# Performance work log

Hardware: AMD Instinct MI355X
Metric: run time of the kernel (lower is better)

Reference implementation:

```python
import jax, jax.numpy as jnp
import numpy as np

B, L, HID = 4, 1024, 2048
H, DK, DV, KS = 16, 128, 128, 4
KEY_DIM, VAL_DIM = H * DK, H * DV
CONV_DIM = 2 * KEY_DIM + VAL_DIM
EPS = 1e-6


def setup_inputs() -> dict:
    key = jax.random.key(0)
    ks = jax.random.split(key, 8)
    return {
        "hidden_states": jax.random.normal(ks[0], (B, L, HID), jnp.float32),
        "W_qkvz": jax.random.normal(ks[1], (HID, 2 * KEY_DIM + 2 * VAL_DIM), jnp.float32) * 0.02,
        "W_ba": jax.random.normal(ks[2], (HID, 2 * H), jnp.float32) * 0.02,
        "conv_w": jax.random.normal(ks[3], (CONV_DIM, KS), jnp.float32) * 0.1,
        "conv_b": jnp.zeros((CONV_DIM,), jnp.float32),
        "A_log": jnp.log(jax.random.uniform(ks[4], (H,), jnp.float32, 1e-3, 16.0)),
        "dt_bias": jnp.ones((H,), jnp.float32),
        "norm_w": jnp.ones((DV,), jnp.float32),
        "W_out": jax.random.normal(ks[5], (VAL_DIM, HID), jnp.float32) * 0.02,
    }


def _l2norm(x):
    return x * jax.lax.rsqrt(jnp.sum(x * x, -1, keepdims=True) + EPS)


def _gdn_core(q, k, v, g, beta):
    # q,k: [B,L,H,DK], v: [B,L,H,DV], g,beta: [B,L,H]
    scale = q.shape[-1] ** -0.5

    def step(S, inp):
        qt, kt, vt, gt, bt = inp  # [B,H,*]
        S = S * jnp.exp(gt)[..., None, None]          # per-step gated decay
        v_pred = jnp.einsum('bhk,bhkd->bhd', kt, S)   # read memory at k_t
        delta = (vt - v_pred) * bt[..., None]         # delta-rule update
        S = S + jnp.einsum('bhk,bhd->bhkd', kt, delta)
        o = jnp.einsum('bhk,bhkd->bhd', qt, S) * scale
        return S, o

    S0 = jnp.zeros((q.shape[0], q.shape[2], q.shape[3], v.shape[3]), q.dtype)
    xs = (q.transpose(1, 0, 2, 3), k.transpose(1, 0, 2, 3), v.transpose(1, 0, 2, 3),
          g.transpose(1, 0, 2), beta.transpose(1, 0, 2))
    _, o = jax.lax.scan(step, S0, xs)
    return o.transpose(1, 0, 2, 3)  # [B,L,H,DV]


def reference(hidden_states, W_qkvz, W_ba, conv_w, conv_b, A_log, dt_bias, norm_w, W_out):
    qkvz = hidden_states @ W_qkvz                      # [B,L,2*key+2*val]
    ba = hidden_states @ W_ba                          # [B,L,2H]
    mixed = qkvz[..., :CONV_DIM]
    z = qkvz[..., CONV_DIM:].reshape(B, L, H, DV)
    b_, a_ = ba[..., :H], ba[..., H:]

    # depthwise causal conv1d (left pad KS-1), no activation (activation=None)
    x = mixed.transpose(0, 2, 1)                       # [B,C,L]
    x = jax.lax.conv_general_dilated(
        x, conv_w[:, None, :], (1,), [(KS - 1, 0)],
        dimension_numbers=('NCH', 'OIH', 'NCH'), feature_group_count=CONV_DIM)
    x = (x + conv_b[None, :, None]).transpose(0, 2, 1)  # [B,L,C]

    q = _l2norm(x[..., :KEY_DIM].reshape(B, L, H, DK))
    k = _l2norm(x[..., KEY_DIM:2 * KEY_DIM].reshape(B, L, H, DK))
    v = x[..., 2 * KEY_DIM:].reshape(B, L, H, DV)

    g = -jnp.exp(A_log)[None, None, :] * jax.nn.softplus(a_ + dt_bias[None, None, :])
    beta = jax.nn.sigmoid(b_)

    o = _gdn_core(q, k, v, g, beta)                    # [B,L,H,DV]

    # gated RMSNorm (norm before gate)
    var = jnp.mean(o * o, -1, keepdims=True)
    o = o * jax.lax.rsqrt(var + EPS) * norm_w * jax.nn.sigmoid(z)
    return o.reshape(B, L, VAL_DIM) @ W_out            # [B,L,HID]
```

## Files before the change

kernel.cpp:

```cpp
#include <hip/hip_runtime.h>

typedef unsigned short u16;
typedef unsigned int u32;
typedef short short8 __attribute__((ext_vector_type(8)));
typedef float float4v __attribute__((ext_vector_type(4)));

#define L_SEQ 1024
#define NB 4
#define NH 16
#define DK 128
#define DV 128
#define HID 2048
#define NQKVZ 8192
#define CONV_DIM 6144
#define GDN_SCALE 0.08838834764831845f

static __device__ __forceinline__ float bf2f(u16 u) {
    union { u32 i; float f; } x; x.i = ((u32)u) << 16; return x.f;
}
static __device__ __forceinline__ u16 f2bf(float f) {
    union { float f; u32 u; } x; x.f = f;
    u32 r = x.u + 0x7FFF + ((x.u >> 16) & 1);
    return (u16)(r >> 16);
}

union FragU { short8 v; uint4 u; };

#define GLOAD_LDS16(g, l)                                        \
    __builtin_amdgcn_global_load_lds(                            \
        (const __attribute__((address_space(1))) void*)(g),      \
        (__attribute__((address_space(3))) void*)(l), 16, 0, 0)

__global__ __launch_bounds__(256) void f32_to_bf16(
    const float* __restrict__ in, u16* __restrict__ out) {
    long i = ((long)blockIdx.x * 256 + threadIdx.x) * 8;
    float4 a = *(const float4*)(in + i);
    float4 b = *(const float4*)(in + i + 4);
    u16 tmp[8];
    tmp[0] = f2bf(a.x); tmp[1] = f2bf(a.y); tmp[2] = f2bf(a.z); tmp[3] = f2bf(a.w);
    tmp[4] = f2bf(b.x); tmp[5] = f2bf(b.y); tmp[6] = f2bf(b.z); tmp[7] = f2bf(b.w);
    *(uint4*)(out + i) = *(const uint4*)tmp;
}

__global__ __launch_bounds__(256) void transpose_f32_bf16(
    const float* __restrict__ in, u16* __restrict__ out, int R, int C) {
    __shared__ float tile[32][33];
    int bx = blockIdx.x, by = blockIdx.y;
    int c = threadIdx.x & 31;
    int r0 = threadIdx.x >> 5;
#pragma unroll
    for (int i = 0; i < 4; i++) {
        int r = r0 + i * 8;
        tile[r][c] = in[(long)(by * 32 + r) * C + bx * 32 + c];
    }
    __syncthreads();
#pragma unroll
    for (int i = 0; i < 4; i++) {
        int r = r0 + i * 8;
        out[(long)(bx * 32 + r) * R + by * 32 + c] = f2bf(tile[c][r]);
    }
}

__global__ __launch_bounds__(256) void convw_transpose(
    const float* __restrict__ w, float* __restrict__ wT) {
    int c = blockIdx.x * 256 + threadIdx.x;
    float4 v = *(const float4*)(w + c * 4);
    wT[0 * CONV_DIM + c] = v.x;
    wT[1 * CONV_DIM + c] = v.y;
    wT[2 * CONV_DIM + c] = v.z;
    wT[3 * CONV_DIM + c] = v.w;
}

#define BM 128
#define BN 128
#define BKK 32

static __device__ __forceinline__ void store_out(u16* p, float v)  { *p = f2bf(v); }
static __device__ __forceinline__ void store_out(float* p, float v){ *p = v; }

template <typename OutT>
__global__ __launch_bounds__(256) void gemm_abT(
    const u16* __restrict__ A, const u16* __restrict__ BT,
    OutT* __restrict__ C, int M, int N, int K) {
    __shared__ u16 As[BM * BKK];
    __shared__ u16 Bs[BN * BKK];
    int t = threadIdx.x;
    int lane = t & 63;
    int w = t >> 6;
    int wm = (w & 1) * 64;
    int wn = (w >> 1) * 64;
    int l15 = lane & 15;
    int quad = lane >> 4;
    long blockM = (long)blockIdx.y * BM;
    long blockN = (long)blockIdx.x * BN;

    float4v acc[4][4];
#pragma unroll
    for (int i = 0; i < 4; i++)
#pragma unroll
        for (int j = 0; j < 4; j++) acc[i][j] = (float4v){0.f, 0.f, 0.f, 0.f};

    const u16* Ab = A + blockM * K;
    const u16* Bb = BT + blockN * K;

    const int r0 = t >> 2,         c0 = (t & 3) * 8;
    const int r1 = (t + 256) >> 2, c1 = ((t + 256) & 3) * 8;
    u16* As0 = As + t * 8;         u16* As1 = As + (t + 256) * 8;
    u16* Bs0 = Bs + t * 8;         u16* Bs1 = Bs + (t + 256) * 8;
    const u16* Ag0 = Ab + (long)r0 * K + c0;
    const u16* Ag1 = Ab + (long)r1 * K + c1;
    const u16* Bg0 = Bb + (long)r0 * K + c0;
    const u16* Bg1 = Bb + (long)r1 * K + c1;

    for (int k0 = 0; k0 < K; k0 += BKK) {
        __syncthreads();
        GLOAD_LDS16(Ag0 + k0, As0);
        GLOAD_LDS16(Ag1 + k0, As1);
        GLOAD_LDS16(Bg0 + k0, Bs0);
        GLOAD_LDS16(Bg1 + k0, Bs1);
        __syncthreads();

        FragU fa[4], fb[4];
#pragma unroll
        for (int i = 0; i < 4; i++) {
            fa[i].u = *(const uint4*)(As + (wm + i * 16 + l15) * BKK + quad * 8);
            fb[i].u = *(const uint4*)(Bs + (wn + i * 16 + l15) * BKK + quad * 8);
        }
#pragma unroll
        for (int i = 0; i < 4; i++)
#pragma unroll
            for (int j = 0; j < 4; j++)
                acc[i][j] = __builtin_amdgcn_mfma_f32_16x16x32_bf16(
                    fa[i].v, fb[j].v, acc[i][j], 0, 0, 0);
    }

#pragma unroll
    for (int i = 0; i < 4; i++) {
        long mrow = blockM + wm + i * 16 + quad * 4;
#pragma unroll
        for (int j = 0; j < 4; j++) {
            long col = blockN + wn + j * 16 + l15;
#pragma unroll
            for (int r = 0; r < 4; r++) {
                store_out(&C[(mrow + r) * N + col], acc[i][j][r]);
            }
        }
    }
}

#define G1_LDSU 32768

__global__ __launch_bounds__(512, 2) void gemm1_8ph(
    const u16* __restrict__ A, const u16* __restrict__ BT,
    u16* __restrict__ C) {
    const int K = HID, N = NQKVZ;
    __shared__ __align__(16) u16 lds[2 * G1_LDSU];

    int t = threadIdx.x;
    int lane = t & 63, w = t >> 6, l15 = lane & 15, quad = lane >> 4;
    int wm = w & 1, wn = w >> 1;

    int orig = blockIdx.x;
    int wg = (orig & 7) * 64 + (orig >> 3);
    int p = wg >> 6, q = wg & 63;
    long blockM = (long)((p >> 2) * 8 + (q >> 3)) * 256;
    long blockN = (long)((p & 3) * 8 + (q & 7)) * 256;

    int srow = t >> 3;
    int scol = ((t & 7) ^ (srow & 7)) * 8;
    const u16* Ast = A + (blockM + srow) * (long)K + scol;
    const u16* Bst = BT + (blockN + srow) * (long)K + scol;

#define STA(db, qq, T) GLOAD_LDS16(Ast + (long)(qq) * 64 * K + (T) * 64,      \
                                   lds + (db) * G1_LDSU + (qq) * 4096 + t * 8)
#define STB(db, qq, T) GLOAD_LDS16(Bst + (long)(qq) * 64 * K + (T) * 64,      \
                                   lds + (db) * G1_LDSU + 16384 + (qq) * 4096 + t * 8)

    const int rowA0 = (wm * 128 + l15) * 64;
    const int rowB0 = 16384 + (wn * 64 + l15) * 64;
    const int cs0 = ((quad) ^ (l15 & 7)) * 8;
    const int cs1 = ((4 + quad) ^ (l15 & 7)) * 8;

    float4v acc[8][4];
#pragma unroll
    for (int mi = 0; mi < 8; mi++)
#pragma unroll
        for (int nj = 0; nj < 4; nj++) acc[mi][nj] = (float4v){0.f, 0.f, 0.f, 0.f};

    STA(0, 0, 0); STA(0, 1, 0); STA(0, 2, 0); STA(0, 3, 0);
    STB(0, 0, 0); STB(0, 1, 0); STB(0, 2, 0); STB(0, 3, 0);
    STA(1, 0, 1); STA(1, 2, 1);
    asm volatile("s_waitcnt vmcnt(2)" ::: "memory");
    __builtin_amdgcn_s_barrier();

    FragU bA[4][2], bB0[2][2], bB1[2][2];

    for (int g = 0; g < 32; ++g) {
        const int c = g & 1, db = c ^ 1;
        const u16* sb = lds + c * G1_LDSU;

#pragma unroll
        for (int i = 0; i < 4; i++) {
            bA[i][0].u = *(const uint4*)(sb + rowA0 + i * 1024 + cs0);
            bA[i][1].u = *(const uint4*)(sb + rowA0 + i * 1024 + cs1);
        }
#pragma unroll
        for (int j = 0; j < 2; j++) {
            bB0[j][0].u = *(const uint4*)(sb + rowB0 + j * 1024 + cs0);
            bB0[j][1].u = *(const uint4*)(sb + rowB0 + j * 1024 + cs1);
        }
        if (g + 1 < 32) { STA(db, 1, g + 1); STA(db, 3, g + 1); }
        __builtin_amdgcn_s_barrier();
        asm volatile("s_waitcnt lgkmcnt(0)" ::: "memory");
        __builtin_amdgcn_s_setprio(1);
#pragma unroll
        for (int i = 0; i < 4; i++)
#pragma unroll
            for (int j = 0; j < 2; j++) {
                acc[i][j] = __builtin_amdgcn_mfma_f32_16x16x32_bf16(
                    bA[i][0].v, bB0[j][0].v, acc[i][j], 0, 0, 0);
                acc[i][j] = __builtin_amdgcn_mfma_f32_16x16x32_bf16(
                    bA[i][1].v, bB0[j][1].v, acc[i][j], 0, 0, 0);
            }
        __builtin_amdgcn_s_setprio(0);

#pragma unroll
        for (int j = 0; j < 2; j++) {
            bB1[j][0].u = *(const uint4*)(sb + rowB0 + (2 + j) * 1024 + cs0);
            bB1[j][1].u = *(const uint4*)(sb + rowB0 + (2 + j) * 1024 + cs1);
        }
        if (g + 1 < 32) { STB(db, 0, g + 1); STB(db, 1, g + 1); }
        __builtin_amdgcn_s_barrier();
        asm volatile("s_waitcnt lgkmcnt(0)" ::: "memory");
        __builtin_amdgcn_s_setprio(1);
#pragma unroll
        for (int i = 0; i < 4; i++)
#pragma unroll
            for (int j = 0; j < 2; j++) {
                acc[i][2 + j] = __builtin_amdgcn_mfma_f32_16x16x32_bf16(
                    bA[i][0].v, bB1[j][0].v, acc[i][2 + j], 0, 0, 0);
                acc[i][2 + j] = __builtin_amdgcn_mfma_f32_16x16x32_bf16(
                    bA[i][1].v, bB1[j][1].v, acc[i][2 + j], 0, 0, 0);
            }
        __builtin_amdgcn_s_setprio(0);

#pragma unroll
        for (int i = 0; i < 4; i++) {
            bA[i][0].u = *(const uint4*)(sb + rowA0 + (4 + i) * 1024 + cs0);
            bA[i][1].u = *(const uint4*)(sb + rowA0 + (4 + i) * 1024 + cs1);
        }
        if (g + 1 < 32) { STB(db, 2, g + 1); STB(db, 3, g + 1); }
        __builtin_amdgcn_s_barrier();
        asm volatile("s_waitcnt lgkmcnt(0)" ::: "memory");
        __builtin_amdgcn_s_setprio(1);
#pragma unroll
        for (int i = 0; i < 4; i++)
#pragma unroll
            for (int j = 0; j < 2; j++) {
                acc[4 + i][j] = __builtin_amdgcn_mfma_f32_16x16x32_bf16(
                    bA[i][0].v, bB0[j][0].v, acc[4 + i][j], 0, 0, 0);
                acc[4 + i][j] = __builtin_amdgcn_mfma_f32_16x16x32_bf16(
                    bA[i][1].v, bB0[j][1].v, acc[4 + i][j], 0, 0, 0);
            }
        __builtin_amdgcn_s_setprio(0);

        if (g + 2 < 32) { STA(c, 0, g + 2); STA(c, 2, g + 2); }
        __builtin_amdgcn_s_barrier();
        __builtin_amdgcn_s_setprio(1);
#pragma unroll
        for (int i = 0; i < 4; i++)
#pragma unroll
            for (int j = 0; j < 2; j++) {
                acc[4 + i][2 + j] = __builtin_amdgcn_mfma_f32_16x16x32_bf16(
                    bA[i][0].v, bB1[j][0].v, acc[4 + i][2 + j], 0, 0, 0);
                acc[4 + i][2 + j] = __builtin_amdgcn_mfma_f32_16x16x32_bf16(
                    bA[i][1].v, bB1[j][1].v, acc[4 + i][2 + j], 0, 0, 0);
            }
        __builtin_amdgcn_s_setprio(0);

        if (g < 30)       { asm volatile("s_waitcnt vmcnt(2)" ::: "memory"); }
        else if (g == 30) { asm volatile("s_waitcnt vmcnt(0)" ::: "memory"); }
        __builtin_amdgcn_s_barrier();
    }

#pragma unroll
    for (int mi = 0; mi < 8; mi++) {
        long row0 = blockM + wm * 128 + mi * 16 + quad * 4;
#pragma unroll
        for (int nj = 0; nj < 4; nj++) {
            long col = blockN + wn * 64 + nj * 16 + l15;
#pragma unroll
            for (int r = 0; r < 4; r++)
                C[(row0 + r) * N + col] = f2bf(acc[mi][nj][r]);
        }
    }
#undef STA
#undef STB
}

#define G2_LDSU 24576

__global__ __launch_bounds__(512) void gemm2_2ph(
    const u16* __restrict__ A, const u16* __restrict__ BT,
    float* __restrict__ C) {
    const int K = HID, N = 2048;
    __shared__ __align__(16) u16 lds[2 * G2_LDSU];

    int t = threadIdx.x;
    int lane = t & 63, w = t >> 6, l15 = lane & 15, quad = lane >> 4;
    int wm = w & 1, wn = w >> 1;

    int orig = blockIdx.x;
    int x = orig & 7, q = orig >> 3;
    long blockM = (long)((x >> 2) * 8 + (q >> 2)) * 256;
    long blockN = (long)((x & 3) * 4 + (q & 3)) * 128;

    int srow = t >> 3;
    int scol = ((t & 7) ^ (srow & 7)) * 8;
    const u16* Ast = A + (blockM + srow) * (long)K + scol;
    const u16* Bst = BT + (blockN + srow) * (long)K + scol;

#define STA2(db, qq, T) GLOAD_LDS16(Ast + (long)(qq) * 64 * K + (T) * 64,     \
                                    lds + (db) * G2_LDSU + (qq) * 4096 + t * 8)
#define STB2(db, hh, T) GLOAD_LDS16(Bst + (long)(hh) * 64 * K + (T) * 64,     \
                                    lds + (db) * G2_LDSU + 16384 + (hh) * 4096 + t * 8)

    const int cs0 = ((quad) ^ (l15 & 7)) * 8;
    const int cs1 = ((4 + quad) ^ (l15 & 7)) * 8;
    int offA[8], offB[2];
#pragma unroll
    for (int mi = 0; mi < 8; mi++)
        offA[mi] = (wm * 2 + (mi >> 2)) * 4096 + (((mi & 3) * 16 + l15)) * 64;
#pragma unroll
    for (int nj = 0; nj < 2; nj++)
        offB[nj] = 16384 + (wn >> 1) * 4096 + ((wn & 1) * 32 + nj * 16 + l15) * 64;

    float4v acc[8][2];
#pragma unroll
    for (int mi = 0; mi < 8; mi++)
#pragma unroll
        for (int nj = 0; nj < 2; nj++) acc[mi][nj] = (float4v){0.f, 0.f, 0.f, 0.f};

    STA2(0, 0, 0); STA2(0, 2, 0); STB2(0, 0, 0); STB2(0, 1, 0);
    STA2(0, 1, 0); STA2(0, 3, 0);
    STA2(1, 0, 1); STA2(1, 2, 1); STB2(1, 0, 1); STB2(1, 1, 1);
    asm volatile("s_waitcnt vmcnt(6)" ::: "memory");
    __builtin_amdgcn_s_barrier();

    FragU fA[4][2], fB[2][2];

    for (int g = 0; g < 32; ++g) {
        const int c = g & 1, db = c ^ 1;
        const u16* sb = lds + c * G2_LDSU;

#pragma unroll
        for (int i = 0; i < 4; i++) {
            fA[i][0].u = *(const uint4*)(sb + offA[i] + cs0);
            fA[i][1].u = *(const uint4*)(sb + offA[i] + cs1);
        }
#pragma unroll
        for (int j = 0; j < 2; j++) {
            fB[j][0].u = *(const uint4*)(sb + offB[j] + cs0);
            fB[j][1].u = *(const uint4*)(sb + offB[j] + cs1);
        }
        if (g < 31) { STA2(db, 1, g + 1); STA2(db, 3, g + 1); }
        asm volatile("s_waitcnt lgkmcnt(8)" ::: "memory");
        __builtin_amdgcn_s_barrier();
        __builtin_amdgcn_s_setprio(1);
#pragma unroll
        for (int i = 0; i < 4; i++)
#pragma unroll
            for (int j = 0; j < 2; j++) {
                acc[i][j] = __builtin_amdgcn_mfma_f32_16x16x32_bf16(
                    fA[i][0].v, fB[j][0].v, acc[i][j], 0, 0, 0);
                acc[i][j] = __builtin_amdgcn_mfma_f32_16x16x32_bf16(
                    fA[i][1].v, fB[j][1].v, acc[i][j], 0, 0, 0);
            }
        __builtin_amdgcn_s_setprio(0);

        if (g < 31) { asm volatile("s_waitcnt vmcnt(6)" ::: "memory"); }
        else        { asm volatile("s_waitcnt vmcnt(0)" ::: "memory"); }
        __builtin_amdgcn_s_barrier();
        if (g < 30) { STA2(c, 0, g + 2); STA2(c, 2, g + 2);
                      STB2(c, 0, g + 2); STB2(c, 1, g + 2); }
#pragma unroll
        for (int i = 0; i < 4; i++) {
            fA[i][0].u = *(const uint4*)(sb + offA[4 + i] + cs0);
            fA[i][1].u = *(const uint4*)(sb + offA[4 + i] + cs1);
        }
        __builtin_amdgcn_s_setprio(1);
#pragma unroll
        for (int i = 0; i < 4; i++)
#pragma unroll
            for (int j = 0; j < 2; j++) {
                acc[4 + i][j] = __builtin_amdgcn_mfma_f32_16x16x32_bf16(
                    fA[i][0].v, fB[j][0].v, acc[4 + i][j], 0, 0, 0);
                acc[4 + i][j] = __builtin_amdgcn_mfma_f32_16x16x32_bf16(
                    fA[i][1].v, fB[j][1].v, acc[4 + i][j], 0, 0, 0);
            }
        __builtin_amdgcn_s_setprio(0);

        if (g < 30)       { asm volatile("s_waitcnt vmcnt(6)" ::: "memory"); }
        else if (g == 30) { asm volatile("s_waitcnt vmcnt(2)" ::: "memory"); }
        if (g < 31) __builtin_amdgcn_s_barrier();
    }

#pragma unroll
    for (int mi = 0; mi < 8; mi++) {
        long row0 = blockM + wm * 128 + mi * 16 + quad * 4;
#pragma unroll
        for (int nj = 0; nj < 2; nj++) {
            long col = blockN + wn * 32 + nj * 16 + l15;
#pragma unroll
            for (int r = 0; r < 4; r++)
                C[(row0 + r) * N + col] = acc[mi][nj][r];
        }
    }
#undef STA2
#undef STB2
}

__global__ __launch_bounds__(256) void ba_gemm(
    const u16* __restrict__ hsb, const u16* __restrict__ WbaTb,
    const float* __restrict__ A_log, const float* __restrict__ dtb,
    float* __restrict__ gout, float* __restrict__ bout) {
    __shared__ u16 As[2][32 * 32];
    __shared__ u16 Bs[2][32 * 32];
    int t = threadIdx.x;
    int lane = t & 63, w = t >> 6, l15 = lane & 15, quad = lane >> 4;
    long blockM = (long)blockIdx.x * 32;

    float4v acc = (float4v){0.f, 0.f, 0.f, 0.f};

    int sidx = t & 127;
    const u16* Sg = (t < 128)
        ? hsb + (blockM + (sidx >> 2)) * (long)HID + (sidx & 3) * 8
        : WbaTb + (long)(sidx >> 2) * HID + (sidx & 3) * 8;
    u16* Sl0 = (t < 128) ? As[0] + sidx * 8 : Bs[0] + sidx * 8;
    u16* Sl1 = (t < 128) ? As[1] + sidx * 8 : Bs[1] + sidx * 8;

    GLOAD_LDS16(Sg + 0, Sl0);
    GLOAD_LDS16(Sg + 32, Sl1);

    const int wr = (w >> 1) * 16, wc = (w & 1) * 16;

    for (int k0 = 0; k0 < HID; k0 += 32) {
        int buf = (k0 >> 5) & 1;
        if (k0 < HID - 64) { asm volatile("s_waitcnt vmcnt(1)" ::: "memory"); }
        else               { asm volatile("s_waitcnt vmcnt(0)" ::: "memory"); }
        __builtin_amdgcn_s_barrier();
        FragU fa, fb;
        fa.u = *(const uint4*)(As[buf] + (wr + l15) * 32 + quad * 8);
        fb.u = *(const uint4*)(Bs[buf] + (wc + l15) * 32 + quad * 8);
        asm volatile("s_waitcnt lgkmcnt(0)" ::: "memory");
        __builtin_amdgcn_sched_barrier(0);
        __builtin_amdgcn_s_barrier();
        if (k0 + 64 < HID) GLOAD_LDS16(Sg + k0 + 64, buf ? Sl1 : Sl0);
        acc = __builtin_amdgcn_mfma_f32_16x16x32_bf16(fa.v, fb.v, acc, 0, 0, 0);
    }

    {
        int n = wc + l15;
#pragma unroll
        for (int r = 0; r < 4; r++) {
            long m = blockM + wr + quad * 4 + r;
            int b = (int)(m >> 10), l = (int)(m & 1023);
            float v = acc[r];
            if (n < 16) {
                bout[((long)(b * NH + n)) * L_SEQ + l] = 1.f / (1.f + expf(-v));
            } else {
                int h = n - 16;
                float x = v + dtb[h];
                float sp = (x > 20.f) ? x : log1pf(expf(x));
                gout[((long)(b * NH + h)) * L_SEQ + l] = -expf(A_log[h]) * sp;
            }
        }
    }
}

__global__ __launch_bounds__(256) void conv_qkv(
    const u16* __restrict__ qkvz, const float* __restrict__ wT,
    const float* __restrict__ conv_b,
    u16* __restrict__ qs, u16* __restrict__ ks, u16* __restrict__ vs) {
    int orig = blockIdx.x;
    int bl = ((orig & 7) << 9) + (orig >> 3);
    int b = bl >> 10, l = bl & 1023;
    int t = threadIdx.x;
    const int ok3 = (l >= 3), ok2 = (l >= 2), ok1 = (l >= 1);
    const int h = t >> 4;
    const int d = (t & 15) * 8;

#pragma unroll
    for (int pass = 0; pass < 3; pass++) {
        int c = pass * 2048 + t * 8;
        long rowbase = (long)(b * L_SEQ + l) * NQKVZ + c;
        uint4 x0 = *(const uint4*)(qkvz + rowbase);
        uint4 x1 = ok1 ? *(const uint4*)(qkvz + rowbase - 1L * NQKVZ) : (uint4){0, 0, 0, 0};
        uint4 x2 = ok2 ? *(const uint4*)(qkvz + rowbase - 2L * NQKVZ) : (uint4){0, 0, 0, 0};
        uint4 x3 = ok3 ? *(const uint4*)(qkvz + rowbase - 3L * NQKVZ) : (uint4){0, 0, 0, 0};
        float w3[8], w2[8], w1[8], w0[8], bb[8];
        *(float4*)&w3[0] = *(const float4*)(wT + 0 * CONV_DIM + c);
        *(float4*)&w3[4] = *(const float4*)(wT + 0 * CONV_DIM + c + 4);
        *(float4*)&w2[0] = *(const float4*)(wT + 1 * CONV_DIM + c);
        *(float4*)&w2[4] = *(const float4*)(wT + 1 * CONV_DIM + c + 4);
        *(float4*)&w1[0] = *(const float4*)(wT + 2 * CONV_DIM + c);
        *(float4*)&w1[4] = *(const float4*)(wT + 2 * CONV_DIM + c + 4);
        *(float4*)&w0[0] = *(const float4*)(wT + 3 * CONV_DIM + c);
        *(float4*)&w0[4] = *(const float4*)(wT + 3 * CONV_DIM + c + 4);
        *(float4*)&bb[0] = *(const float4*)(conv_b + c);
        *(float4*)&bb[4] = *(const float4*)(conv_b + c + 4);
        const u16* p0 = (const u16*)&x0;
        const u16* p1 = (const u16*)&x1;
        const u16* p2 = (const u16*)&x2;
        const u16* p3 = (const u16*)&x3;
        float v[8];
#pragma unroll
        for (int j = 0; j < 8; j++) {
            float a = bb[j] + bf2f(p0[j]) * w0[j];
            if (ok1) a += bf2f(p1[j]) * w1[j];
            if (ok2) a += bf2f(p2[j]) * w2[j];
            if (ok3) a += bf2f(p3[j]) * w3[j];
            v[j] = a;
        }
        u16 outv[8];
        if (pass < 2) {
            float s = 0.f;
#pragma unroll
            for (int j = 0; j < 8; j++) s += v[j] * v[j];
            s += __shfl_xor(s, 1);
            s += __shfl_xor(s, 2);
            s += __shfl_xor(s, 4);
            s += __shfl_xor(s, 8);
            float r = rsqrtf(s + 1e-6f);
#pragma unroll
            for (int j = 0; j < 8; j++) outv[j] = f2bf(v[j] * r);
            u16* dst = (pass == 0) ? qs : ks;
            *(uint4*)&dst[(((long)(b * NH + h)) * L_SEQ + l) * DK + d] = *(const uint4*)outv;
        } else {
#pragma unroll
            for (int j = 0; j < 8; j++) outv[j] = f2bf(v[j]);
            *(uint4*)&vs[(((long)(b * NH + h)) * L_SEQ + l) * DV + d] = *(const uint4*)outv;
        }
    }
}

__global__ __launch_bounds__(256) void gdn_prep(
    const u16* __restrict__ ks_g, const u16* __restrict__ qs_g,
    const float* __restrict__ g_g, const float* __restrict__ b_g,
    u16* __restrict__ Tbuf, u16* __restrict__ Pbuf,
    u16* __restrict__ wbq, u16* __restrict__ qlq, u16* __restrict__ kdq,
    float* __restrict__ gam_g) {
    int cid = blockIdx.x;
    int bh = cid >> 4;
    int ch = cid & 15;
    long rowbase = (long)bh * L_SEQ + ch * 64;
    int t = threadIdx.x;
    int lane = t & 63, w = t >> 6, l15 = lane & 15, quad = lane >> 4;

    __shared__ u16 Kl[64 * 136];
    __shared__ u16 Ql[64 * 136];
    __shared__ float Am[64 * 66];
    __shared__ float Tm[64 * 66];
    __shared__ float Tt[32 * 33];
    __shared__ float Gs[64], lamL[64], betaL[64], dlL[64];

    {
        int row = t >> 2, seg = (t & 3) * 32;
        const u16* ksrc = ks_g + (rowbase + row) * DK + seg;
        const u16* qsrc = qs_g + (rowbase + row) * DK + seg;
        *(uint4*)&Kl[row * 136 + seg]      = *(const uint4*)ksrc;
        *(uint4*)&Kl[row * 136 + seg + 8]  = *(const uint4*)(ksrc + 8);
        *(uint4*)&Kl[row * 136 + seg + 16] = *(const uint4*)(ksrc + 16);
        *(uint4*)&Kl[row * 136 + seg + 24] = *(const uint4*)(ksrc + 24);
        *(uint4*)&Ql[row * 136 + seg]      = *(const uint4*)qsrc;
        *(uint4*)&Ql[row * 136 + seg + 8]  = *(const uint4*)(qsrc + 8);
        *(uint4*)&Ql[row * 136 + seg + 16] = *(const uint4*)(qsrc + 16);
        *(uint4*)&Ql[row * 136 + seg + 24] = *(const uint4*)(qsrc + 24);
        if (t < 64) Gs[t] = g_g[rowbase + t];
        else if (t < 128) betaL[t - 64] = b_g[rowbase + t - 64];
    }
    __syncthreads();
    if (t < 64) {
        float gv = Gs[t];
#pragma unroll
        for (int off = 1; off < 64; off <<= 1) {
            float n = __shfl_up(gv, off);
            if (lane >= off) gv += n;
        }
        Gs[t] = gv;
    }
    __syncthreads();
    if (t < 64) {
        float G63 = Gs[63];
        float lm = expf(Gs[t]);
        lamL[t] = lm;
        dlL[t] = expf(G63 - Gs[t]);
        if (t == 0) gam_g[cid] = expf(G63);
    }
    float4v accKK[4], accQK[4];
#pragma unroll
    for (int tj = 0; tj < 4; tj++) {
        accKK[tj] = (float4v){0.f, 0.f, 0.f, 0.f};
        accQK[tj] = (float4v){0.f, 0.f, 0.f, 0.f};
    }
#pragma unroll
    for (int k0 = 0; k0 < 128; k0 += 32) {
        FragU ka, qa;
        ka.u = *(const uint4*)&Kl[(w * 16 + l15) * 136 + k0 + quad * 8];
        qa.u = *(const uint4*)&Ql[(w * 16 + l15) * 136 + k0 + quad * 8];
#pragma unroll
        for (int tj = 0; tj < 4; tj++) {
            FragU kb;
            kb.u = *(const uint4*)&Kl[(tj * 16 + l15) * 136 + k0 + quad * 8];
            accKK[tj] = __builtin_amdgcn_mfma_f32_16x16x32_bf16(ka.v, kb.v, accKK[tj], 0, 0, 0);
            accQK[tj] = __builtin_amdgcn_mfma_f32_16x16x32_bf16(qa.v, kb.v, accQK[tj], 0, 0, 0);
        }
    }
    __syncthreads();
#pragma unroll
    for (int tj = 0; tj < 4; tj++) {
#pragma unroll
        for (int r = 0; r < 4; r++) {
            int ti_ = w * 16 + quad * 4 + r;
            int j = tj * 16 + l15;
            float e = (j <= ti_) ? expf(Gs[ti_] - Gs[j]) : 0.f;
            Am[ti_ * 66 + j] = (j < ti_) ? betaL[ti_] * e * accKK[tj][r] : 0.f;
            Pbuf[(long)cid * 4096 + ti_ * 64 + j] =
                (j <= ti_) ? f2bf(GDN_SCALE * e * accQK[tj][r]) : (u16)0;
        }
    }
    {
        int row = t >> 2, seg = (t & 3) * 32;
        float sw = -betaL[row] * lamL[row];
        float sq = GDN_SCALE * lamL[row];
#pragma unroll
        for (int c0 = 0; c0 < 32; c0 += 8) {
            u16 wt[8], qt2[8];
#pragma unroll
            for (int j2 = 0; j2 < 8; j2++) {
                wt[j2]  = f2bf(sw * bf2f(Kl[row * 136 + seg + c0 + j2]));
                qt2[j2] = f2bf(sq * bf2f(Ql[row * 136 + seg + c0 + j2]));
            }
            *(uint4*)&wbq[(long)cid * 8192 + row * 128 + seg + c0] = *(uint4*)wt;
            *(uint4*)&qlq[(long)cid * 8192 + row * 128 + seg + c0] = *(uint4*)qt2;
        }
    }
    {
        int k = t & 127, t0b = (t >> 7) * 32;
#pragma unroll
        for (int t0 = 0; t0 < 32; t0 += 8) {
            u16 tmp[8];
#pragma unroll
            for (int j2 = 0; j2 < 8; j2++)
                tmp[j2] = f2bf(dlL[t0b + t0 + j2] * bf2f(Kl[(t0b + t0 + j2) * 136 + k]));
            *(uint4*)&kdq[(long)cid * 8192 + k * 64 + t0b + t0] = *(uint4*)tmp;
        }
    }
    __syncthreads();
    if (t < 32) {
        int c = t;
        for (int i = 0; i < 32; i++) {
            float s = (i == c) ? 1.f : 0.f;
            for (int j = 0; j < i; j++) s -= Am[i * 66 + j] * Tm[j * 66 + c];
            Tm[i * 66 + c] = s;
        }
    } else if (t >= 64 && t < 96) {
        int c = 32 + (t - 64);
        for (int i = 32; i < 64; i++) {
            float s = (i == c) ? 1.f : 0.f;
            for (int j = 32; j < i; j++) s -= Am[i * 66 + j] * Tm[j * 66 + c];
            Tm[i * 66 + c] = s;
        }
    } else if (t >= 128 && t < 192) {
        int idx = t - 128;
        for (int kk = 0; kk < 16; kk++) {
            int e = idx * 16 + kk;
            Tm[(e >> 5) * 66 + 32 + (e & 31)] = 0.f;
        }
    }
    __syncthreads();
    {
        int e0 = t * 4;
#pragma unroll
        for (int kk = 0; kk < 4; kk++) {
            int e = e0 + kk; int i = e >> 5, c = e & 31;
            float s = 0.f;
            for (int j = 0; j < 32; j++) s += Am[(32 + i) * 66 + j] * Tm[j * 66 + c];
            Tt[i * 33 + c] = s;
        }
    }
    __syncthreads();
    {
        int e0 = t * 4;
#pragma unroll
        for (int kk = 0; kk < 4; kk++) {
            int e = e0 + kk; int i = e >> 5, c = e & 31;
            float s = 0.f;
            for (int j = 0; j < 32; j++) s -= Tm[(32 + i) * 66 + 32 + j] * Tt[j * 33 + c];
            Tm[(32 + i) * 66 + c] = s;
        }
    }
    __syncthreads();
    {
        int row = t >> 2, c0 = (t & 3) * 16;
        u16 tmp[16];
#pragma unroll
        for (int i = 0; i < 16; i++) tmp[i] = f2bf(Tm[row * 66 + c0 + i]);
        *(uint4*)&Tbuf[(long)cid * 4096 + row * 64 + c0]     = *(uint4*)tmp;
        *(uint4*)&Tbuf[(long)cid * 4096 + row * 64 + c0 + 8] = *(uint4*)(tmp + 8);
    }
}

__global__ __launch_bounds__(256) void gdn_chunk(
    const u16* __restrict__ vs_g, const float* __restrict__ b_g,
    const u16* __restrict__ Tq, const u16* __restrict__ Pq,
    const u16* __restrict__ wbq, const u16* __restrict__ qlq,
    const u16* __restrict__ kdq, const float* __restrict__ gam_g,
    float* __restrict__ o_g) {
    int orig = blockIdx.x;
    int bid = ((orig & 7) << 6) + (orig >> 3);
    int dc = bid & 7;
    int bh = bid >> 3;
    int b = bh >> 4, h = bh & 15;
    int t = threadIdx.x;
    int lane = t & 63, w = t >> 6, l15 = lane & 15, quad = lane >> 4;

    __shared__ u16 s0h[16 * 136], s0l[16 * 136];
    __shared__ float vO[64 * 20];
    __shared__ u16 rhsT[16 * 72], DT[16 * 72];

    float4v S0r[2];
    S0r[0] = (float4v){0.f, 0.f, 0.f, 0.f};
    S0r[1] = (float4v){0.f, 0.f, 0.f, 0.f};

    const int orow = t >> 2, oseg = (t & 3) * 4;

    for (int ch = 0; ch < 16; ch++) {
        int cid = bh * 16 + ch;
        long rowbase = (long)bh * L_SEQ + ch * 64;
        float gam = gam_g[cid];

        const u16* wbp = wbq + (long)cid * 8192 + (w * 16 + l15) * 128 + quad * 8;
        uint4 wbf0 = *(const uint4*)(wbp);
        uint4 wbf1 = *(const uint4*)(wbp + 32);
        uint4 wbf2 = *(const uint4*)(wbp + 64);
        uint4 wbf3 = *(const uint4*)(wbp + 96);

        if (ch > 0) {
            float4 a = *(const float4*)&vO[orow * 20 + oseg];
            float* d2 = o_g + (((long)b * L_SEQ + (ch - 1) * 64 + orow) * 16 + h) * 128L
                        + dc * 16 + oseg;
            *(float4*)d2 = a;
        }
        {
            float beta = b_g[rowbase + orow];
            uint2 vv = *(const uint2*)(vs_g + (rowbase + orow) * DV + dc * 16 + oseg);
            const u16* vp = (const u16*)&vv;
#pragma unroll
            for (int j2 = 0; j2 < 4; j2++)
                vO[orow * 20 + oseg + j2] = beta * bf2f(vp[j2]);
        }
#pragma unroll
        for (int ktl = 0; ktl < 2; ktl++) {
            int kc = (2 * w + ktl) * 16 + l15;
#pragma unroll
            for (int r = 0; r < 4; r++) {
                float x = S0r[ktl][r];
                u16 hi = f2bf(x);
                float lo = x - bf2f(hi);
                s0h[(quad * 4 + r) * 136 + kc] = hi;
                s0l[(quad * 4 + r) * 136 + kc] = f2bf(lo);
            }
        }
        __syncthreads();

        const u16* Tp = Tq + (long)cid * 4096 + (w * 16 + l15) * 64 + quad * 8;
        uint4 Tf0 = *(const uint4*)(Tp);
        uint4 Tf1 = *(const uint4*)(Tp + 32);
        {
            float4v acc;
#pragma unroll
            for (int r = 0; r < 4; r++)
                acc[r] = vO[(w * 16 + quad * 4 + r) * 20 + l15];
            uint4 wbf[4] = {wbf0, wbf1, wbf2, wbf3};
#pragma unroll
            for (int k0 = 0; k0 < 4; k0++) {
                FragU a, bh_, bl_;
                a.u = wbf[k0];
                bh_.u = *(const uint4*)&s0h[l15 * 136 + k0 * 32 + quad * 8];
                acc = __builtin_amdgcn_mfma_f32_16x16x32_bf16(a.v, bh_.v, acc, 0, 0, 0);
                bl_.u = *(const uint4*)&s0l[l15 * 136 + k0 * 32 + quad * 8];
                acc = __builtin_amdgcn_mfma_f32_16x16x32_bf16(a.v, bl_.v, acc, 0, 0, 0);
            }
            u16 tmp[4] = {f2bf(acc[0]), f2bf(acc[1]), f2bf(acc[2]), f2bf(acc[3])};
            *(uint2*)&rhsT[l15 * 72 + w * 16 + quad * 4] = *(uint2*)tmp;
        }
        __syncthreads();

        const u16* qlp = qlq + (long)cid * 8192 + (w * 16 + l15) * 128 + quad * 8;
        uint4 qlf0 = *(const uint4*)(qlp);
        uint4 qlf1 = *(const uint4*)(qlp + 32);
        uint4 qlf2 = *(const uint4*)(qlp + 64);
        uint4 qlf3 = *(const uint4*)(qlp + 96);
        const u16* Pp = Pq + (long)cid * 4096 + (w * 16 + l15) * 64 + quad * 8;
        uint4 Pf0 = *(const uint4*)(Pp);
        uint4 Pf1 = *(const uint4*)(Pp + 32);
        {
            float4v acc = (float4v){0.f, 0.f, 0.f, 0.f};
            uint4 Tf[2] = {Tf0, Tf1};
#pragma unroll
            for (int k0 = 0; k0 < 2; k0++) {
                FragU a, b_;
                a.u = Tf[k0];
                b_.u = *(const uint4*)&rhsT[l15 * 72 + k0 * 32 + quad * 8];
                acc = __builtin_amdgcn_mfma_f32_16x16x32_bf16(a.v, b_.v, acc, 0, 0, 0);
            }
            u16 tmp[4] = {f2bf(acc[0]), f2bf(acc[1]), f2bf(acc[2]), f2bf(acc[3])};
            *(uint2*)&DT[l15 * 72 + w * 16 + quad * 4] = *(uint2*)tmp;
        }
        __syncthreads();

        uint4 kdf[2][2];
#pragma unroll
        for (int ktl = 0; ktl < 2; ktl++) {
            const u16* kdp = kdq + (long)cid * 8192 + ((2 * w + ktl) * 16 + l15) * 64 + quad * 8;
            kdf[ktl][0] = *(const uint4*)(kdp);
            kdf[ktl][1] = *(const uint4*)(kdp + 32);
        }
        {
            float4v acc = (float4v){0.f, 0.f, 0.f, 0.f};
            uint4 qlf[4] = {qlf0, qlf1, qlf2, qlf3};
#pragma unroll
            for (int k0 = 0; k0 < 4; k0++) {
                FragU a, bh_, bl_;
                a.u = qlf[k0];
                bh_.u = *(const uint4*)&s0h[l15 * 136 + k0 * 32 + quad * 8];
                acc = __builtin_amdgcn_mfma_f32_16x16x32_bf16(a.v, bh_.v, acc, 0, 0, 0);
                bl_.u = *(const uint4*)&s0l[l15 * 136 + k0 * 32 + quad * 8];
                acc = __builtin_amdgcn_mfma_f32_16x16x32_bf16(a.v, bl_.v, acc, 0, 0, 0);
            }
            uint4 Pf[2] = {Pf0, Pf1};
#pragma unroll
            for (int k0 = 0; k0 < 2; k0++) {
                FragU a, b_;
                a.u = Pf[k0];
                b_.u = *(const uint4*)&DT[l15 * 72 + k0 * 32 + quad * 8];
                acc = __builtin_amdgcn_mfma_f32_16x16x32_bf16(a.v, b_.v, acc, 0, 0, 0);
            }
#pragma unroll
            for (int r = 0; r < 4; r++)
                vO[(w * 16 + quad * 4 + r) * 20 + l15] = acc[r];
        }
#pragma unroll
        for (int ktl = 0; ktl < 2; ktl++) {
            float4v acc = S0r[ktl];
#pragma unroll
            for (int r = 0; r < 4; r++) acc[r] *= gam;
#pragma unroll
            for (int t0 = 0; t0 < 2; t0++) {
                FragU a, b_;
                a.u = *(const uint4*)&DT[l15 * 72 + t0 * 32 + quad * 8];
                b_.u = kdf[ktl][t0];
                acc = __builtin_amdgcn_mfma_f32_16x16x32_bf16(a.v, b_.v, acc, 0, 0, 0);
            }
            S0r[ktl] = acc;
        }
        __syncthreads();
    }
    {
        float4 a = *(const float4*)&vO[orow * 20 + oseg];
        float* d2 = o_g + (((long)b * L_SEQ + 15 * 64 + orow) * 16 + h) * 128L
                    + dc * 16 + oseg;
        *(float4*)d2 = a;
    }
}

__global__ __launch_bounds__(128) void gated_norm(
    const float* __restrict__ o, const u16* __restrict__ qkvz,
    const float* __restrict__ norm_w, u16* __restrict__ A2) {
    int bid = blockIdx.x;
    int t = threadIdx.x;
    float ov = o[(long)bid * 128 + t];
    float s = ov * ov;
#pragma unroll
    for (int off = 32; off > 0; off >>= 1) s += __shfl_down(s, off);
    __shared__ float ws2[2];
    if ((t & 63) == 0) ws2[t >> 6] = s;
    __syncthreads();
    float tot = ws2[0] + ws2[1];
    float rinv = rsqrtf(tot * (1.f / 128.f) + 1e-6f);
    int bl = bid >> 4, h = bid & 15;
    float z = bf2f(qkvz[(long)bl * NQKVZ + CONV_DIM + h * 128 + t]);
    float sig = 1.f / (1.f + expf(-z));
    float val = ov * rinv * norm_w[t] * sig;
    A2[(long)bl * 2048 + h * 128 + t] = f2bf(val);
}

extern "C" void kernel_launch(void* const* d_in, const int* in_sizes, int n_in,
                              void* d_out, int out_size, void* d_ws, size_t ws_size,
                              hipStream_t stream) {
    const float* hs    = (const float*)d_in[0];
    const float* Wqkvz = (const float*)d_in[1];
    const float* Wba   = (const float*)d_in[2];
    const float* convw = (const float*)d_in[3];
    const float* convb = (const float*)d_in[4];
    const float* A_log = (const float*)d_in[5];
    const float* dtb   = (const float*)d_in[6];
    const float* normw = (const float*)d_in[7];
    const float* Wout  = (const float*)d_in[8];

    char* ws = (char*)d_ws;
    size_t off = 0;
    auto alloc = [&](size_t bytes) {
        size_t o = off;
        off = (off + bytes + 255) & ~(size_t)255;
        return o;
    };
    size_t r0 = alloc((size_t)NQKVZ * HID * 2);
    size_t r1 = alloc((size_t)4096 * HID * 2);
    u16*   WqkvzT = (u16*)(ws + r0);
    float* os     = (float*)(ws + r0);
    u16*   hsb    = (u16*)(ws + r1);
    u16*   A2     = (u16*)(ws + r1);
    u16*   qkvz   = (u16*)(ws + alloc((size_t)4096 * NQKVZ * 2));
    u16*   qs     = (u16*)(ws + alloc((size_t)64 * L_SEQ * DK * 2));
    u16*   ks     = (u16*)(ws + alloc((size_t)64 * L_SEQ * DK * 2));
    u16*   vs     = (u16*)(ws + alloc((size_t)64 * L_SEQ * DV * 2));
    float* gs     = (float*)(ws + alloc((size_t)64 * L_SEQ * 4));
    float* bs     = (float*)(ws + alloc((size_t)64 * L_SEQ * 4));
    u16*   WoutT  = (u16*)(ws + alloc((size_t)HID * 2048 * 2));
    u16*   WbaTb  = (u16*)(ws + alloc((size_t)32 * HID * 2));
    u16*   Tbuf   = (u16*)(ws + alloc((size_t)1024 * 4096 * 2));
    u16*   Pbuf   = (u16*)(ws + alloc((size_t)1024 * 4096 * 2));
    u16*   wbq    = (u16*)(ws + alloc((size_t)1024 * 8192 * 2));
    u16*   qlq    = (u16*)(ws + alloc((size_t)1024 * 8192 * 2));
    u16*   kdq    = (u16*)(ws + alloc((size_t)1024 * 8192 * 2));
    float* gamb   = (float*)(ws + alloc((size_t)1024 * 4));
    float* convwT = (float*)(ws + alloc((size_t)4 * CONV_DIM * 4));

    hipLaunchKernelGGL(f32_to_bf16, dim3(4096), dim3(256), 0, stream, hs, hsb);
    hipLaunchKernelGGL(transpose_f32_bf16, dim3(NQKVZ / 32, HID / 32), dim3(256), 0, stream,
                       Wqkvz, WqkvzT, HID, NQKVZ);
    hipLaunchKernelGGL(transpose_f32_bf16, dim3(2048 / 32, 2048 / 32), dim3(256), 0, stream,
                       Wout, WoutT, 2048, 2048);
    hipLaunchKernelGGL(transpose_f32_bf16, dim3(1, HID / 32), dim3(256), 0, stream,
                       Wba, WbaTb, HID, 32);
    hipLaunchKernelGGL(convw_transpose, dim3(CONV_DIM / 256), dim3(256), 0, stream,
                       convw, convwT);

    hipLaunchKernelGGL(gemm1_8ph, dim3(512), dim3(512), 0, stream,
                       hsb, WqkvzT, qkvz);

    hipLaunchKernelGGL(ba_gemm, dim3(128), dim3(256), 0, stream,
                       hsb, WbaTb, A_log, dtb, gs, bs);

    hipLaunchKernelGGL(conv_qkv, dim3(4096), dim3(256), 0, stream,
                       qkvz, convwT, convb, qs, ks, vs);

    hipLaunchKernelGGL(gdn_prep, dim3(1024), dim3(256), 0, stream,
                       ks, qs, gs, bs, Tbuf, Pbuf, wbq, qlq, kdq, gamb);

    hipLaunchKernelGGL(gdn_chunk, dim3(512), dim3(256), 0, stream,
                       vs, bs, Tbuf, Pbuf, wbq, qlq, kdq, gamb, os);

    hipLaunchKernelGGL(gated_norm, dim3(4096 * NH), dim3(128), 0, stream,
                       os, qkvz, normw, A2);

    hipLaunchKernelGGL(gemm2_2ph, dim3(256), dim3(512), 0, stream,
                       A2, WoutT, (float*)d_out);
}
```

Baseline: 505.0 us.

## Fuse input prep kernels into one launch and use lighter LDS barriers

```diff
diff --git a/kernel.cpp b/kernel.cpp
--- a/kernel.cpp
+++ b/kernel.cpp
@@ -31,120 +31,79 @@
         (const __attribute__((address_space(1))) void*)(g),      \
         (__attribute__((address_space(3))) void*)(l), 16, 0, 0)
 
-__global__ __launch_bounds__(256) void f32_to_bf16(
-    const float* __restrict__ in, u16* __restrict__ out) {
-    long i = ((long)blockIdx.x * 256 + threadIdx.x) * 8;
-    float4 a = *(const float4*)(in + i);
-    float4 b = *(const float4*)(in + i + 4);
-    u16 tmp[8];
-    tmp[0] = f2bf(a.x); tmp[1] = f2bf(a.y); tmp[2] = f2bf(a.z); tmp[3] = f2bf(a.w);
-    tmp[4] = f2bf(b.x); tmp[5] = f2bf(b.y); tmp[6] = f2bf(b.z); tmp[7] = f2bf(b.w);
-    *(uint4*)(out + i) = *(const uint4*)tmp;
-}
-
-__global__ __launch_bounds__(256) void transpose_f32_bf16(
-    const float* __restrict__ in, u16* __restrict__ out, int R, int C) {
-    __shared__ float tile[32][33];
-    int bx = blockIdx.x, by = blockIdx.y;
-    int c = threadIdx.x & 31;
-    int r0 = threadIdx.x >> 5;
+#define LBAR() do {                                              \
+    asm volatile("s_waitcnt lgkmcnt(0)" ::: "memory");           \
+    __builtin_amdgcn_s_barrier();                                \
+    __builtin_amdgcn_sched_barrier(0); } while (0)
+
+static __device__ __forceinline__ void transpose64(
+    const float* __restrict__ in, u16* __restrict__ out, int R, int C,
+    int bx, int by, float* tile, int t) {
 #pragma unroll
     for (int i = 0; i < 4; i++) {
-        int r = r0 + i * 8;
-        tile[r][c] = in[(long)(by * 32 + r) * C + bx * 32 + c];
+        int r = (t >> 4) + i * 16;
+        int c4 = (t & 15) * 4;
+        float4 v = *(const float4*)(in + (long)(by * 64 + r) * C + bx * 64 + c4);
+        tile[r * 65 + c4 + 0] = v.x;
+        tile[r * 65 + c4 + 1] = v.y;
+        tile[r * 65 + c4 + 2] = v.z;
+        tile[r * 65 + c4 + 3] = v.w;
     }
     __syncthreads();
 #pragma unroll
-    for (int i = 0; i < 4; i++) {
-        int r = r0 + i * 8;
-        out[(long)(bx * 32 + r) * R + by * 32 + c] = f2bf(tile[c][r]);
-    }
-}
-
-__global__ __launch_bounds__(256) void convw_transpose(
-    const float* __restrict__ w, float* __restrict__ wT) {
-    int c = blockIdx.x * 256 + threadIdx.x;
-    float4 v = *(const float4*)(w + c * 4);
-    wT[0 * CONV_DIM + c] = v.x;
-    wT[1 * CONV_DIM + c] = v.y;
-    wT[2 * CONV_DIM + c] = v.z;
-    wT[3 * CONV_DIM + c] = v.w;
-}
-
-#define BM 128
-#define BN 128
-#define BKK 32
-
-static __device__ __forceinline__ void store_out(u16* p, float v)  { *p = f2bf(v); }
-static __device__ __forceinline__ void store_out(float* p, float v){ *p = v; }
-
-template <typename OutT>
-__global__ __launch_bounds__(256) void gemm_abT(
-    const u16* __restrict__ A, const u16* __restrict__ BT,
-    OutT* __restrict__ C, int M, int N, int K) {
-    __shared__ u16 As[BM * BKK];
-    __shared__ u16 Bs[BN * BKK];
-    int t = threadIdx.x;
-    int lane = t & 63;
-    int w = t >> 6;
-    int wm = (w & 1) * 64;
-    int wn = (w >> 1) * 64;
-    int l15 = lane & 15;
-    int quad = lane >> 4;
-    long blockM = (long)blockIdx.y * BM;
-    long blockN = (long)blockIdx.x * BN;
-
-    float4v acc[4][4];
-#pragma unroll
-    for (int i = 0; i < 4; i++)
-#pragma unroll
-        for (int j = 0; j < 4; j++) acc[i][j] = (float4v){0.f, 0.f, 0.f, 0.f};
-
-    const u16* Ab = A + blockM * K;
-    const u16* Bb = BT + blockN * K;
-
-    const int r0 = t >> 2,         c0 = (t & 3) * 8;
-    const int r1 = (t + 256) >> 2, c1 = ((t + 256) & 3) * 8;
-    u16* As0 = As + t * 8;         u16* As1 = As + (t + 256) * 8;
-    u16* Bs0 = Bs + t * 8;         u16* Bs1 = Bs + (t + 256) * 8;
-    const u16* Ag0 = Ab + (long)r0 * K + c0;
-    const u16* Ag1 = Ab + (long)r1 * K + c1;
-    const u16* Bg0 = Bb + (long)r0 * K + c0;
-    const u16* Bg1 = Bb + (long)r1 * K + c1;
-
-    for (int k0 = 0; k0 < K; k0 += BKK) {
+    for (int p = 0; p < 2; p++) {
+        int oc = (t >> 3) + p * 32;
+        int orb = (t & 7) * 8;
+        u16 vals[8];
+#pragma unroll
+        for (int k = 0; k < 8; k++) vals[k] = f2bf(tile[(orb + k) * 65 + oc]);
+        *(uint4*)(out + (long)(bx * 64 + oc) * R + by * 64 + orb) = *(const uint4*)vals;
+    }
+}
+
+__global__ __launch_bounds__(256) void prep_all(
+    const float* __restrict__ hs, u16* __restrict__ hsb,
+    const float* __restrict__ Wqkvz, u16* __restrict__ WqkvzT,
+    const float* __restrict__ Wout, u16* __restrict__ WoutT,
+    const float* __restrict__ Wba, u16* __restrict__ WbaTb,
+    const float* __restrict__ convw, float* __restrict__ convwT) {
+    __shared__ float tile[64 * 65];
+    int id = blockIdx.x, t = threadIdx.x;
+    if (id < 4096) {
+        long i = ((long)id * 256 + t) * 8;
+        float4 a = *(const float4*)(hs + i);
+        float4 b = *(const float4*)(hs + i + 4);
+        u16 tmp[8];
+        tmp[0] = f2bf(a.x); tmp[1] = f2bf(a.y); tmp[2] = f2bf(a.z); tmp[3] = f2bf(a.w);
+        tmp[4] = f2bf(b.x); tmp[5] = f2bf(b.y); tmp[6] = f2bf(b.z); tmp[7] = f2bf(b.w);
+        *(uint4*)(hsb + i) = *(const uint4*)tmp;
+    } else if (id < 8192) {
+        int k = id - 4096;
+        transpose64(Wqkvz, WqkvzT, HID, NQKVZ, k & 127, k >> 7, tile, t);
+    } else if (id < 9216) {
+        int k = id - 8192;
+        transpose64(Wout, WoutT, 2048, 2048, k & 31, k >> 5, tile, t);
+    } else if (id < 9280) {
+        int by = id - 9216;
+        int c = t & 31, r0 = t >> 5;
+#pragma unroll
+        for (int i = 0; i < 4; i++) {
+            int r = r0 + i * 8;
+            tile[r * 33 + c] = Wba[(long)(by * 32 + r) * 32 + c];
+        }
         __syncthreads();
-        GLOAD_LDS16(Ag0 + k0, As0);
-        GLOAD_LDS16(Ag1 + k0, As1);
-        GLOAD_LDS16(Bg0 + k0, Bs0);
-        GLOAD_LDS16(Bg1 + k0, Bs1);
-        __syncthreads();
-
-        FragU fa[4], fb[4];
 #pragma unroll
         for (int i = 0; i < 4; i++) {
-            fa[i].u = *(const uint4*)(As + (wm + i * 16 + l15) * BKK + quad * 8);
-            fb[i].u = *(const uint4*)(Bs + (wn + i * 16 + l15) * BKK + quad * 8);
-        }
-#pragma unroll
-        for (int i = 0; i < 4; i++)
-#pragma unroll
-            for (int j = 0; j < 4; j++)
-                acc[i][j] = __builtin_amdgcn_mfma_f32_16x16x32_bf16(
-                    fa[i].v, fb[j].v, acc[i][j], 0, 0, 0);
-    }
-
-#pragma unroll
-    for (int i = 0; i < 4; i++) {
-        long mrow = blockM + wm + i * 16 + quad * 4;
-#pragma unroll
-        for (int j = 0; j < 4; j++) {
-            long col = blockN + wn + j * 16 + l15;
-#pragma unroll
-            for (int r = 0; r < 4; r++) {
-                store_out(&C[(mrow + r) * N + col], acc[i][j][r]);
-            }
-        }
+            int r = r0 + i * 8;
+            WbaTb[(long)r * HID + by * 32 + c] = f2bf(tile[c * 33 + r]);
+        }
+    } else {
+        int c = (id - 9280) * 256 + t;
+        float4 v = *(const float4*)(convw + c * 4);
+        convwT[0 * CONV_DIM + c] = v.x;
+        convwT[1 * CONV_DIM + c] = v.y;
+        convwT[2 * CONV_DIM + c] = v.z;
+        convwT[3 * CONV_DIM + c] = v.w;
     }
 }
 
@@ -579,7 +538,7 @@
         if (t < 64) Gs[t] = g_g[rowbase + t];
         else if (t < 128) betaL[t - 64] = b_g[rowbase + t - 64];
     }
-    __syncthreads();
+    LBAR();
     if (t < 64) {
         float gv = Gs[t];
 #pragma unroll
@@ -589,7 +548,7 @@
         }
         Gs[t] = gv;
     }
-    __syncthreads();
+    LBAR();
     if (t < 64) {
         float G63 = Gs[63];
         float lm = expf(Gs[t]);
@@ -616,7 +575,7 @@
             accQK[tj] = __builtin_amdgcn_mfma_f32_16x16x32_bf16(qa.v, kb.v, accQK[tj], 0, 0, 0);
         }
     }
-    __syncthreads();
+    LBAR();
 #pragma unroll
     for (int tj = 0; tj < 4; tj++) {
 #pragma unroll
@@ -656,7 +615,7 @@
             *(uint4*)&kdq[(long)cid * 8192 + k * 64 + t0b + t0] = *(uint4*)tmp;
         }
     }
-    __syncthreads();
+    LBAR();
     if (t < 32) {
         int c = t;
         for (int i = 0; i < 32; i++) {
@@ -678,7 +637,7 @@
             Tm[(e >> 5) * 66 + 32 + (e & 31)] = 0.f;
         }
     }
-    __syncthreads();
+    LBAR();
     {
         int e0 = t * 4;
 #pragma unroll
@@ -689,7 +648,7 @@
             Tt[i * 33 + c] = s;
         }
     }
-    __syncthreads();
+    LBAR();
     {
         int e0 = t * 4;
 #pragma unroll
@@ -700,7 +659,7 @@
             Tm[(32 + i) * 66 + c] = s;
         }
     }
-    __syncthreads();
+    LBAR();
     {
         int row = t >> 2, c0 = (t & 3) * 16;
         u16 tmp[16];
@@ -772,7 +731,7 @@
                 s0l[(quad * 4 + r) * 136 + kc] = f2bf(lo);
             }
         }
-        __syncthreads();
+        LBAR();
 
         const u16* Tp = Tq + (long)cid * 4096 + (w * 16 + l15) * 64 + quad * 8;
         uint4 Tf0 = *(const uint4*)(Tp);
@@ -795,7 +754,7 @@
             u16 tmp[4] = {f2bf(acc[0]), f2bf(acc[1]), f2bf(acc[2]), f2bf(acc[3])};
             *(uint2*)&rhsT[l15 * 72 + w * 16 + quad * 4] = *(uint2*)tmp;
         }
-        __syncthreads();
+        LBAR();
 
         const u16* qlp = qlq + (long)cid * 8192 + (w * 16 + l15) * 128 + quad * 8;
         uint4 qlf0 = *(const uint4*)(qlp);
@@ -818,7 +777,7 @@
             u16 tmp[4] = {f2bf(acc[0]), f2bf(acc[1]), f2bf(acc[2]), f2bf(acc[3])};
             *(uint2*)&DT[l15 * 72 + w * 16 + quad * 4] = *(uint2*)tmp;
         }
-        __syncthreads();
+        LBAR();
 
         uint4 kdf[2][2];
 #pragma unroll
@@ -865,7 +824,7 @@
             }
             S0r[ktl] = acc;
         }
-        __syncthreads();
+        LBAR();
     }
     {
         float4 a = *(const float4*)&vO[orow * 20 + oseg];
@@ -938,14 +897,8 @@
     float* gamb   = (float*)(ws + alloc((size_t)1024 * 4));
     float* convwT = (float*)(ws + alloc((size_t)4 * CONV_DIM * 4));
 
-    hipLaunchKernelGGL(f32_to_bf16, dim3(4096), dim3(256), 0, stream, hs, hsb);
-    hipLaunchKernelGGL(transpose_f32_bf16, dim3(NQKVZ / 32, HID / 32), dim3(256), 0, stream,
-                       Wqkvz, WqkvzT, HID, NQKVZ);
-    hipLaunchKernelGGL(transpose_f32_bf16, dim3(2048 / 32, 2048 / 32), dim3(256), 0, stream,
-                       Wout, WoutT, 2048, 2048);
-    hipLaunchKernelGGL(transpose_f32_bf16, dim3(1, HID / 32), dim3(256), 0, stream,
-                       Wba, WbaTb, HID, 32);
-    hipLaunchKernelGGL(convw_transpose, dim3(CONV_DIM / 256), dim3(256), 0, stream,
+    hipLaunchKernelGGL(prep_all, dim3(9304), dim3(256), 0, stream,
+                       hs, hsb, Wqkvz, WqkvzT, Wout, WoutT, Wba, WbaTb,
                        convw, convwT);
 
     hipLaunchKernelGGL(gemm1_8ph, dim3(512), dim3(512), 0, stream,
```

After: 494.7 us. 1.02x faster.
